# Optimization experiments

Hardware: AMD Instinct MI355X
Metric: run time of the kernel (lower is better)

The kernel has to match this reference:

```python
import jax, jax.numpy as jnp
import numpy as np
from jax import lax

B, C, H, W = 2, 128, 96, 96
K = 3
KK = K * K
EPS = 1e-5


def setup_inputs() -> dict:
    key = jax.random.key(0)
    ks = jax.random.split(key, 4)
    d = {"hu": jax.random.normal(ks[0], (B, C, H, W), jnp.float32)}
    for i in range(3):
        k = jax.random.split(ks[i + 1], 7)
        d["off_w%d" % (i + 1)] = jax.random.normal(k[0], (3 * KK, C, K, K), jnp.float32) * 0.01
        d["off_b%d" % (i + 1)] = jax.random.normal(k[1], (3 * KK,), jnp.float32) * 0.01
        d["w%d" % (i + 1)] = jax.random.normal(k[2], (C, C, K, K), jnp.float32) / np.float32(np.sqrt(C * KK))
        d["g%d" % (i + 1)] = jax.random.uniform(k[3], (C,), jnp.float32) + 0.5
        d["b%d" % (i + 1)] = jax.random.normal(k[4], (C,), jnp.float32) * 0.1
        d["m%d" % (i + 1)] = jax.random.normal(k[5], (C,), jnp.float32) * 0.1
        d["v%d" % (i + 1)] = jax.random.uniform(k[6], (C,), jnp.float32) + 0.5
    return d


def _mod_deform_conv(x, w, offset, mask, dilation):
    # x: [B,C,H,W]; offset: [B,2*KK,H,W] (dy,dx interleaved per kernel tap);
    # mask: [B,KK,H,W] (already sigmoid'ed). Zero padding outside the image.
    Hh, Ww = x.shape[2], x.shape[3]
    pad = dilation * (K - 1) // 2
    ky = jnp.repeat(jnp.arange(K), K).astype(x.dtype)  # [KK] row of each tap
    kx = jnp.tile(jnp.arange(K), K).astype(x.dtype)    # [KK] col of each tap
    gy = (jnp.arange(Hh, dtype=x.dtype) - pad)[None, :, None] + (ky * dilation)[:, None, None]  # [KK,H,1]
    gx = (jnp.arange(Ww, dtype=x.dtype) - pad)[None, None, :] + (kx * dilation)[:, None, None]  # [KK,1,W]
    off = offset.reshape(x.shape[0], KK, 2, Hh, Ww)
    py = gy[None] + off[:, :, 0]  # [B,KK,H,W] sampling row
    px = gx[None] + off[:, :, 1]  # [B,KK,H,W] sampling col

    def sample_one(xb, pyb, pxb, mb):
        # xb: [C,H,W]; pyb/pxb/mb: [KK,H,W]
        y0 = jnp.floor(pyb)
        x0 = jnp.floor(pxb)
        ly = pyb - y0
        lx = pxb - x0
        acc = jnp.zeros((xb.shape[0],) + pyb.shape, xb.dtype)
        for dy, wy in ((0, 1.0 - ly), (1, ly)):
            for dx, wx in ((0, 1.0 - lx), (1, lx)):
                yi = y0 + dy
                xi = x0 + dx
                valid = (yi >= 0) & (yi <= Hh - 1) & (xi >= 0) & (xi <= Ww - 1)
                yc = jnp.clip(yi, 0, Hh - 1).astype(jnp.int32)
                xc = jnp.clip(xi, 0, Ww - 1).astype(jnp.int32)
                v = xb[:, yc, xc]  # gather -> [C,KK,H,W]
                acc = acc + v * (wy * wx * valid.astype(xb.dtype))[None]
        return acc * mb[None]  # modulation

    sampled = jax.vmap(sample_one)(x, py, px, mask)  # [B,C,KK,H,W]
    return jnp.einsum('bckhw,ock->bohw', sampled, w.reshape(w.shape[0], w.shape[1], KK))


def _block(x, off_w, off_b, w, g, b, m, v, dilation):
    pad = dilation * (K - 1) // 2
    om = lax.conv_general_dilated(
        x, off_w, (1, 1), [(pad, pad), (pad, pad)],
        rhs_dilation=(dilation, dilation),
        dimension_numbers=('NCHW', 'OIHW', 'NCHW')) + off_b[None, :, None, None]
    offset = om[:, :2 * KK]
    mask = jax.nn.sigmoid(om[:, 2 * KK:])
    y = _mod_deform_conv(x, w, offset, mask, dilation)
    scale = (g / jnp.sqrt(v + EPS))[None, :, None, None]  # BN (inference form)
    y = (y - m[None, :, None, None]) * scale + b[None, :, None, None]
    return jax.nn.relu(y)


def reference(hu, off_w1, off_b1, w1, g1, b1, m1, v1,
              off_w2, off_b2, w2, g2, b2, m2, v2,
              off_w3, off_b3, w3, g3, b3, m3, v3):
    a1 = _block(hu, off_w1, off_b1, w1, g1, b1, m1, v1, 2) + hu
    a2 = _block(a1, off_w2, off_b2, w2, g2, b2, m2, v2, 4) + a1
    a3 = _block(a2, off_w3, off_b3, w3, g3, b3, m3, v3, 8) + a2
    return a3
```

## Files before the change

kernel.cpp:

```cpp
#include <hip/hip_runtime.h>
#include <math.h>

constexpr int Bn  = 2;
constexpr int Cn  = 128;
constexpr int Hn  = 96;
constexpr int Wn  = 96;
constexpr int HWn = Hn * Wn;
constexpr int CHWn = Cn * HWn;
constexpr int KCn = Cn * 9;
constexpr float EPSn = 1e-5f;
constexpr int KPAD = 1160;

typedef short bf16x8 __attribute__((ext_vector_type(8)));
typedef float f32x4  __attribute__((ext_vector_type(4)));

static __device__ inline short f2bf(float f) {
    union { float f; unsigned u; } v; v.f = f;
    unsigned r = v.u + 0x7fff + ((v.u >> 16) & 1);
    return (short)(r >> 16);
}
static __device__ inline unsigned pack2(float a, float b) {
    unsigned r;
    asm("v_cvt_pk_bf16_f32 %0, %1, %2" : "=v"(r) : "v"(a), "v"(b));
    return r;
}
static __device__ inline float bflo(unsigned u) { return __int_as_float(u << 16); }
static __device__ inline float bfhi(unsigned u) { return __int_as_float(u & 0xffff0000u); }

__global__ __launch_bounds__(256) void cvt_w_all(
    const float* __restrict__ w1, const float* __restrict__ w2,
    const float* __restrict__ w3, short* __restrict__ wbs)
{
    const int bid = blockIdx.x;
    const int stage = bid / 576;
    const float* w = (stage == 0) ? w1 : (stage == 1) ? w2 : w3;
    int t = (bid - stage * 576) * 256 + threadIdx.x;
    int e = t & 7, l = (t >> 3) & 63, rest = t >> 9;
    int j = rest % 36, g = rest / 36;
    int lr = l & 15, lq = l >> 4;
    int o = g * 16 + lr;
    int kidx = j * 32 + lq * 8 + e;
    int k = kidx >> 7, c = kidx & 127;
    wbs[stage * Cn * KCn + t] = f2bf(w[o * KCn + c * 9 + k]);
}

__global__ __launch_bounds__(256) void cvt_ow_all(
    const float* __restrict__ w1, const float* __restrict__ w2,
    const float* __restrict__ w3, short* __restrict__ owbs)
{
    const int bid = blockIdx.x;
    const int stage = bid / 144;
    const float* ow = (stage == 0) ? w1 : (stage == 1) ? w2 : w3;
    int t = (bid - stage * 144) * 256 + threadIdx.x;
    int e = t & 7, l = (t >> 3) & 63, rest = t >> 9;
    int kk = rest % 9, wvv = rest / 9;
    int mh = wvv & 1, ks = wvv >> 1;
    int lr = l & 15, lq = l >> 4;
    int o = mh * 16 + lr;
    int kidx = ks * 288 + kk * 32 + lq * 8 + e;
    int k = kidx >> 7, c = kidx & 127;
    owbs[stage * 32 * KCn + t] = (o < 27) ? f2bf(ow[o * KCn + c * 9 + k]) : (short)0;
}

__global__ __launch_bounds__(256) void nchw2nhwc(
    const float* __restrict__ x, unsigned short* __restrict__ xTb)
{
    __shared__ float Tl[128][65];
    const int t = threadIdx.x;
    const int pix0 = blockIdx.x * 64;
    const int b   = pix0 / HWn;
    const int sp0 = pix0 - b * HWn;
    const float* xb = x + b * CHWn + sp0 + (t & 63);
    const int c0 = t >> 6;
#pragma unroll 8
    for (int i = 0; i < 32; ++i) {
        const int c = c0 + 4 * i;
        Tl[c][t & 63] = xb[c * HWn];
    }
    __syncthreads();
    unsigned short* dstb = xTb + pix0 * 128;
#pragma unroll 8
    for (int i = 0; i < 32; ++i) {
        const int o = t + 256 * i;
        dstb[o] = (unsigned short)f2bf(Tl[o & 127][o >> 7]);
    }
}

__global__ __launch_bounds__(512, 6) void fused_stage(
    const unsigned short* __restrict__ xTb,
    const short* __restrict__ wbs, const short* __restrict__ owbs,
    const float* __restrict__ obv,
    const float* __restrict__ gv, const float* __restrict__ bv,
    const float* __restrict__ mv, const float* __restrict__ vv,
    unsigned short* __restrict__ outTb,
    float* __restrict__ outC, int dil, int last)
{
    __shared__ short S[16 * KPAD];
    __shared__ float offL[16][18];
    __shared__ float maskL[16][9];

    const int t   = threadIdx.x;
    const int l   = t & 63;
    const int wv  = t >> 6;
    const int lh  = l >> 5;
    const int lc  = l & 31;

    const int bid = blockIdx.x;
    const int swz = (bid & 7) * 144 + (bid >> 3);
    const int pix0 = swz * 16;
    const int b   = pix0 / HWn;
    const int sp0 = pix0 - b * HWn;
    const int hy  = sp0 / Wn;
    const int wx0 = sp0 - hy * Wn;
    const int basep = b * HWn;

    bf16x8 oaf[9];
    {
        const short* oarow = owbs + (wv * 9) * 512 + l * 8;
#pragma unroll
        for (int u = 0; u < 9; ++u) oaf[u] = *(const bf16x8*)(oarow + u * 512);
    }

#pragma unroll
    for (int bch = 0; bch < 3; ++bch) {
        uint2 vle[3];
#pragma unroll
        for (int u = 0; u < 3; ++u) {
            const int k  = bch * 3 + u;
            const int pp = wv * 2 + lh;
            const int iy = hy + (k / 3 - 1) * dil;
            const int ix = wx0 + pp + (k % 3 - 1) * dil;
            const bool v = (iy >= 0) && (iy < Hn) && (ix >= 0) && (ix < Wn);
            const int aof = v ? (basep + iy * Wn + ix) : basep;
            uint2 val = ((const uint2*)(xTb + aof * 128))[lc];
            vle[u].x = v ? val.x : 0u;
            vle[u].y = v ? val.y : 0u;
        }
#pragma unroll
        for (int u = 0; u < 3; ++u) {
            const int k  = bch * 3 + u;
            const int pp = wv * 2 + lh;
            ((uint2*)&S[pp * KPAD + k * 128])[lc] = vle[u];
        }
    }
    __syncthreads();

    f32x4 oacc = {0.f, 0.f, 0.f, 0.f};
    {
        const int ks = wv >> 1;
        const short* srow = &S[(l & 15) * KPAD + ks * 288 + ((l >> 4) * 8)];
#pragma unroll
        for (int bch = 0; bch < 3; ++bch) {
            bf16x8 bf[3];
#pragma unroll
            for (int u = 0; u < 3; ++u) bf[u] = *(const bf16x8*)(srow + (bch * 3 + u) * 32);
#pragma unroll
            for (int u = 0; u < 3; ++u)
                oacc = __builtin_amdgcn_mfma_f32_16x16x32_bf16(oaf[bch * 3 + u], bf[u], oacc, 0, 0, 0);
        }
    }
    __syncthreads();
    float* red = (float*)S;
    *(f32x4*)&red[wv * 256 + l * 4] = oacc;
    __syncthreads();
    if (wv < 2) {
        f32x4 s0 = *(const f32x4*)&red[(0 * 2 + wv) * 256 + l * 4];
        f32x4 s1 = *(const f32x4*)&red[(1 * 2 + wv) * 256 + l * 4];
        f32x4 s2 = *(const f32x4*)&red[(2 * 2 + wv) * 256 + l * 4];
        f32x4 s3 = *(const f32x4*)&red[(3 * 2 + wv) * 256 + l * 4];
        f32x4 sm = (s0 + s1) + (s2 + s3);
#pragma unroll
        for (int r = 0; r < 4; ++r) {
            int oc = wv * 16 + ((l >> 4) << 2) + r;
            if (oc < 18) {
                offL[l & 15][oc] = sm[r] + obv[oc];
            } else if (oc < 27) {
                float z = sm[r] + obv[oc];
                maskL[l & 15][oc - 18] = 1.f / (1.f + expf(-z));
            }
        }
    }
    __syncthreads();

    int pw0i = 0, pw1i = 0, pw2i = 0, pw3i = 0, pa0 = 0, pa1 = 0, pdx = 0;
    if (l < 18) {
        const int p = wv * 2 + l / 9;
        const int k = l - 9 * (l / 9);
        const float offy = offL[p][2 * k];
        const float offx = offL[p][2 * k + 1];
        const float m    = maskL[p][k];
        const float py = (float)(hy + (k / 3 - 1) * dil) + offy;
        const float px = (float)(wx0 + p + (k % 3 - 1) * dil) + offx;
        const float y0f = floorf(py), x0f = floorf(px);
        const float ly = py - y0f, lx = px - x0f;
        const int y0 = (int)y0f, x0 = (int)x0f;
        const float yv0 = (y0 >= 0 && y0 < Hn)      ? 1.f : 0.f;
        const float yv1 = (y0 >= -1 && y0 < Hn - 1) ? 1.f : 0.f;
        const float xv0 = (x0 >= 0 && x0 < Wn)      ? 1.f : 0.f;
        const float xv1 = (x0 >= -1 && x0 < Wn - 1) ? 1.f : 0.f;
        const float wy0 = (1.f - ly) * yv0 * m;
        const float wy1 = ly * yv1 * m;
        const float wxa = (1.f - lx) * xv0;
        const float wxb = lx * xv1;
        pw0i = __float_as_int(wy0 * wxa);
        pw1i = __float_as_int(wy0 * wxb);
        pw2i = __float_as_int(wy1 * wxa);
        pw3i = __float_as_int(wy1 * wxb);
        const int y0c = min(max(y0, 0), Hn - 1), y1c = min(max(y0 + 1, 0), Hn - 1);
        const int x0c = min(max(x0, 0), Wn - 1), x1c = min(max(x0 + 1, 0), Wn - 1);
        pa0 = (basep + y0c * Wn + x0c) * 128;
        pa1 = (basep + y1c * Wn + x1c) * 128;
        pdx = (x1c - x0c) * 128;
    }

    bf16x8 daf[6];
    {
        const short* darow = wbs + (wv * 36) * 512 + l * 8;
#pragma unroll
        for (int u = 0; u < 6; ++u) daf[u] = *(const bf16x8*)(darow + u * 512);
    }
    const int pp  = l & 15;
    const int ocb = wv * 16 + ((l >> 4) << 2);
    uint2 resb;
    if (last) {
        resb = *(const uint2*)&xTb[(pix0 + pp) * 128 + ocb];
    } else {
        const int o = t * 4;
        resb = *(const uint2*)&xTb[(pix0 + (o >> 7)) * 128 + (o & 127)];
    }

#pragma unroll
    for (int bch = 0; bch < 6; ++bch) {
        unsigned u00[3], u01[3], u10[3], u11[3];
        float    w00[3], w01[3], w10[3], w11[3];
#pragma unroll
        for (int u = 0; u < 3; ++u) {
            const int i = bch * 3 + u;
            w00[u] = __int_as_float(__builtin_amdgcn_readlane(pw0i, i));
            w01[u] = __int_as_float(__builtin_amdgcn_readlane(pw1i, i));
            w10[u] = __int_as_float(__builtin_amdgcn_readlane(pw2i, i));
            w11[u] = __int_as_float(__builtin_amdgcn_readlane(pw3i, i));
            const int a00 = __builtin_amdgcn_readlane(pa0, i);
            const int a11 = __builtin_amdgcn_readlane(pa1, i);
            const int dxk = __builtin_amdgcn_readlane(pdx, i);
            const unsigned short* xp = xTb + a00;
            const unsigned short* xq = xTb + a11;
            u00[u] = ((const unsigned*)xp)[l];
            u01[u] = ((const unsigned*)(xp + dxk))[l];
            u10[u] = ((const unsigned*)(xq - dxk))[l];
            u11[u] = ((const unsigned*)xq)[l];
        }
#pragma unroll
        for (int u = 0; u < 3; ++u) {
            const int i  = bch * 3 + u;
            const int di = i / 9;
            const int k  = i - di * 9;
            const int ppw = wv * 2 + di;
            float s0 = w00[u] * bflo(u00[u]) + w01[u] * bflo(u01[u])
                     + w10[u] * bflo(u10[u]) + w11[u] * bflo(u11[u]);
            float s1 = w00[u] * bfhi(u00[u]) + w01[u] * bfhi(u01[u])
                     + w10[u] * bfhi(u10[u]) + w11[u] * bfhi(u11[u]);
            ((unsigned*)&S[ppw * KPAD + k * 128])[l] = pack2(s0, s1);
        }
    }
    __syncthreads();

    f32x4 dacc = {0.f, 0.f, 0.f, 0.f};
    {
        const short* darow = wbs + (wv * 36) * 512 + l * 8;
        const short* srow  = &S[(l & 15) * KPAD + ((l >> 4) * 8)];
        {
            bf16x8 bf[6];
#pragma unroll
            for (int u = 0; u < 6; ++u) bf[u] = *(const bf16x8*)(srow + u * 32);
#pragma unroll
            for (int u = 0; u < 6; ++u)
                dacc = __builtin_amdgcn_mfma_f32_16x16x32_bf16(daf[u], bf[u], dacc, 0, 0, 0);
        }
#pragma unroll
        for (int bch = 1; bch < 6; ++bch) {
            bf16x8 af[6], bf[6];
#pragma unroll
            for (int u = 0; u < 6; ++u) af[u] = *(const bf16x8*)(darow + (bch * 6 + u) * 512);
#pragma unroll
            for (int u = 0; u < 6; ++u) bf[u] = *(const bf16x8*)(srow  + (bch * 6 + u) * 32);
#pragma unroll
            for (int u = 0; u < 6; ++u)
                dacc = __builtin_amdgcn_mfma_f32_16x16x32_bf16(af[u], bf[u], dacc, 0, 0, 0);
        }
    }

    if (last) {
        const float rs[4] = {bflo(resb.x), bfhi(resb.x), bflo(resb.y), bfhi(resb.y)};
#pragma unroll
        for (int r = 0; r < 4; ++r) {
            const int oc = ocb + r;
            const float sc = gv[oc] * rsqrtf(vv[oc] + EPSn);
            float y = (dacc[r] - mv[oc]) * sc + bv[oc];
            y = fmaxf(y, 0.f) + rs[r];
            outC[b * CHWn + oc * HWn + sp0 + pp] = y;
        }
    } else {
        __syncthreads();
        float* O = (float*)S;
#pragma unroll
        for (int r = 0; r < 4; ++r) {
            const int oc = ocb + r;
            const float sc = gv[oc] * rsqrtf(vv[oc] + EPSn);
            float y = (dacc[r] - mv[oc]) * sc + bv[oc];
            O[pp * 132 + oc] = fmaxf(y, 0.f);
        }
        __syncthreads();
        const int o  = t * 4;
        const int qp = o >> 7, qc = o & 127;
        f32x4 yv = *(f32x4*)&O[qp * 132 + qc];
        yv[0] += bflo(resb.x);
        yv[1] += bfhi(resb.x);
        yv[2] += bflo(resb.y);
        yv[3] += bfhi(resb.y);
        uint2 pk;
        pk.x = pack2(yv[0], yv[1]);
        pk.y = pack2(yv[2], yv[3]);
        *(uint2*)&outTb[(pix0 + qp) * 128 + qc] = pk;
    }
}

extern "C" void kernel_launch(void* const* d_in, const int* in_sizes, int n_in,
                              void* d_out, int out_size, void* d_ws, size_t ws_size,
                              hipStream_t stream) {
    (void)in_sizes; (void)n_in; (void)out_size; (void)ws_size;

    const float* hu = (const float*)d_in[0];

    short* wbs  = (short*)d_ws;
    short* owbs = wbs + 3 * Cn * KCn;
    unsigned short* T0b = (unsigned short*)(owbs + 3 * 32 * KCn);
    unsigned short* T1b = T0b + Bn * CHWn;

    cvt_w_all<<<3 * 576, 256, 0, stream>>>(
        (const float*)d_in[3], (const float*)d_in[10], (const float*)d_in[17], wbs);
    cvt_ow_all<<<3 * 144, 256, 0, stream>>>(
        (const float*)d_in[1], (const float*)d_in[8], (const float*)d_in[15], owbs);

    nchw2nhwc<<<(Bn * HWn) / 64, 256, 0, stream>>>(hu, T0b);

    const int dils[3] = {2, 4, 8};
    const unsigned short* insb[3] = {T0b, T1b, T0b};
    unsigned short* outsb[3] = {T1b, T0b, nullptr};
    const int nblk = (Bn * HWn) / 16;

    for (int i = 0; i < 3; ++i) {
        const float* obv = (const float*)d_in[2 + 7 * i];
        const float* gv  = (const float*)d_in[4 + 7 * i];
        const float* bv  = (const float*)d_in[5 + 7 * i];
        const float* mv  = (const float*)d_in[6 + 7 * i];
        const float* vv  = (const float*)d_in[7 + 7 * i];
        const int last = (i == 2);

        fused_stage<<<nblk, 512, 0, stream>>>(
            insb[i], wbs + i * Cn * KCn, owbs + i * 32 * KCn, obv,
            gv, bv, mv, vv, outsb[i],
            last ? (float*)d_out : nullptr, dils[i], last);
    }
}
```

Before: 106.3 us.

## Merge prep kernels into one launch and raise fused stage occupancy to 8

The two weight-conversion kernels and the NCHW-to-NHWC transpose are folded into a single prep kernel that branches on block index, cutting two launches. The fused stage kernel moves from launch bounds (512,6) to (512,8). To fit the tighter register budget it preloads fewer offset-conv and deform-conv weight fragments into registers and loads the rest just before use. This trades some extra load latency near the MFMAs for more resident waves. The merged prep kernel also allocates the transpose's shared tile for every block, which may reduce how many weight-conversion blocks fit per CU.

```diff
diff --git a/kernel.cpp b/kernel.cpp
--- a/kernel.cpp
+++ b/kernel.cpp
@@ -27,66 +27,64 @@
 static __device__ inline float bflo(unsigned u) { return __int_as_float(u << 16); }
 static __device__ inline float bfhi(unsigned u) { return __int_as_float(u & 0xffff0000u); }
 
-__global__ __launch_bounds__(256) void cvt_w_all(
+__global__ __launch_bounds__(256) void prep_all(
+    const float* __restrict__ hu,
     const float* __restrict__ w1, const float* __restrict__ w2,
-    const float* __restrict__ w3, short* __restrict__ wbs)
-{
-    const int bid = blockIdx.x;
-    const int stage = bid / 576;
-    const float* w = (stage == 0) ? w1 : (stage == 1) ? w2 : w3;
-    int t = (bid - stage * 576) * 256 + threadIdx.x;
-    int e = t & 7, l = (t >> 3) & 63, rest = t >> 9;
-    int j = rest % 36, g = rest / 36;
-    int lr = l & 15, lq = l >> 4;
-    int o = g * 16 + lr;
-    int kidx = j * 32 + lq * 8 + e;
-    int k = kidx >> 7, c = kidx & 127;
-    wbs[stage * Cn * KCn + t] = f2bf(w[o * KCn + c * 9 + k]);
-}
-
-__global__ __launch_bounds__(256) void cvt_ow_all(
-    const float* __restrict__ w1, const float* __restrict__ w2,
-    const float* __restrict__ w3, short* __restrict__ owbs)
-{
-    const int bid = blockIdx.x;
-    const int stage = bid / 144;
-    const float* ow = (stage == 0) ? w1 : (stage == 1) ? w2 : w3;
-    int t = (bid - stage * 144) * 256 + threadIdx.x;
-    int e = t & 7, l = (t >> 3) & 63, rest = t >> 9;
-    int kk = rest % 9, wvv = rest / 9;
-    int mh = wvv & 1, ks = wvv >> 1;
-    int lr = l & 15, lq = l >> 4;
-    int o = mh * 16 + lr;
-    int kidx = ks * 288 + kk * 32 + lq * 8 + e;
-    int k = kidx >> 7, c = kidx & 127;
-    owbs[stage * 32 * KCn + t] = (o < 27) ? f2bf(ow[o * KCn + c * 9 + k]) : (short)0;
-}
-
-__global__ __launch_bounds__(256) void nchw2nhwc(
-    const float* __restrict__ x, unsigned short* __restrict__ xTb)
+    const float* __restrict__ w3,
+    const float* __restrict__ o1, const float* __restrict__ o2,
+    const float* __restrict__ o3,
+    short* __restrict__ wbs, short* __restrict__ owbs,
+    unsigned short* __restrict__ xTb)
 {
     __shared__ float Tl[128][65];
-    const int t = threadIdx.x;
-    const int pix0 = blockIdx.x * 64;
-    const int b   = pix0 / HWn;
-    const int sp0 = pix0 - b * HWn;
-    const float* xb = x + b * CHWn + sp0 + (t & 63);
-    const int c0 = t >> 6;
+    const int bid = blockIdx.x;
+    if (bid < 1728) {
+        const int stage = bid / 576;
+        const float* w = (stage == 0) ? w1 : (stage == 1) ? w2 : w3;
+        int t = (bid - stage * 576) * 256 + threadIdx.x;
+        int e = t & 7, l = (t >> 3) & 63, rest = t >> 9;
+        int j = rest % 36, g = rest / 36;
+        int lr = l & 15, lq = l >> 4;
+        int o = g * 16 + lr;
+        int kidx = j * 32 + lq * 8 + e;
+        int k = kidx >> 7, c = kidx & 127;
+        wbs[stage * Cn * KCn + t] = f2bf(w[o * KCn + c * 9 + k]);
+    } else if (bid < 2160) {
+        const int rb = bid - 1728;
+        const int stage = rb / 144;
+        const float* ow = (stage == 0) ? o1 : (stage == 1) ? o2 : o3;
+        int t = (rb - stage * 144) * 256 + threadIdx.x;
+        int e = t & 7, l = (t >> 3) & 63, rest = t >> 9;
+        int kk = rest % 9, wvv = rest / 9;
+        int mh = wvv & 1, ks = wvv >> 1;
+        int lr = l & 15, lq = l >> 4;
+        int o = mh * 16 + lr;
+        int kidx = ks * 288 + kk * 32 + lq * 8 + e;
+        int k = kidx >> 7, c = kidx & 127;
+        owbs[stage * 32 * KCn + t] = (o < 27) ? f2bf(ow[o * KCn + c * 9 + k]) : (short)0;
+    } else {
+        const int t = threadIdx.x;
+        const int pix0 = (bid - 2160) * 64;
+        const int b   = pix0 / HWn;
+        const int sp0 = pix0 - b * HWn;
+        const float* xb = hu + b * CHWn + sp0 + (t & 63);
+        const int c0 = t >> 6;
 #pragma unroll 8
-    for (int i = 0; i < 32; ++i) {
-        const int c = c0 + 4 * i;
-        Tl[c][t & 63] = xb[c * HWn];
-    }
-    __syncthreads();
-    unsigned short* dstb = xTb + pix0 * 128;
+        for (int i = 0; i < 32; ++i) {
+            const int c = c0 + 4 * i;
+            Tl[c][t & 63] = xb[c * HWn];
+        }
+        __syncthreads();
+        unsigned short* dstb = xTb + pix0 * 128;
 #pragma unroll 8
-    for (int i = 0; i < 32; ++i) {
-        const int o = t + 256 * i;
-        dstb[o] = (unsigned short)f2bf(Tl[o & 127][o >> 7]);
-    }
-}
-
-__global__ __launch_bounds__(512, 6) void fused_stage(
+        for (int i = 0; i < 32; ++i) {
+            const int o = t + 256 * i;
+            dstb[o] = (unsigned short)f2bf(Tl[o & 127][o >> 7]);
+        }
+    }
+}
+
+__global__ __launch_bounds__(512, 8) void fused_stage(
     const unsigned short* __restrict__ xTb,
     const short* __restrict__ wbs, const short* __restrict__ owbs,
     const float* __restrict__ obv,
@@ -114,11 +112,11 @@
     const int wx0 = sp0 - hy * Wn;
     const int basep = b * HWn;
 
-    bf16x8 oaf[9];
+    bf16x8 oaf[6];
     {
         const short* oarow = owbs + (wv * 9) * 512 + l * 8;
 #pragma unroll
-        for (int u = 0; u < 9; ++u) oaf[u] = *(const bf16x8*)(oarow + u * 512);
+        for (int u = 0; u < 6; ++u) oaf[u] = *(const bf16x8*)(oarow + u * 512);
     }
 
 #pragma unroll
@@ -148,15 +146,26 @@
     f32x4 oacc = {0.f, 0.f, 0.f, 0.f};
     {
         const int ks = wv >> 1;
-        const short* srow = &S[(l & 15) * KPAD + ks * 288 + ((l >> 4) * 8)];
-#pragma unroll
-        for (int bch = 0; bch < 3; ++bch) {
+        const short* oarow = owbs + (wv * 9) * 512 + l * 8;
+        const short* srow  = &S[(l & 15) * KPAD + ks * 288 + ((l >> 4) * 8)];
+#pragma unroll
+        for (int bch = 0; bch < 2; ++bch) {
             bf16x8 bf[3];
 #pragma unroll
             for (int u = 0; u < 3; ++u) bf[u] = *(const bf16x8*)(srow + (bch * 3 + u) * 32);
 #pragma unroll
             for (int u = 0; u < 3; ++u)
                 oacc = __builtin_amdgcn_mfma_f32_16x16x32_bf16(oaf[bch * 3 + u], bf[u], oacc, 0, 0, 0);
+        }
+        {
+            bf16x8 af[3], bf[3];
+#pragma unroll
+            for (int u = 0; u < 3; ++u) af[u] = *(const bf16x8*)(oarow + (6 + u) * 512);
+#pragma unroll
+            for (int u = 0; u < 3; ++u) bf[u] = *(const bf16x8*)(srow + (6 + u) * 32);
+#pragma unroll
+            for (int u = 0; u < 3; ++u)
+                oacc = __builtin_amdgcn_mfma_f32_16x16x32_bf16(af[u], bf[u], oacc, 0, 0, 0);
         }
     }
     __syncthreads();
@@ -213,11 +222,11 @@
         pdx = (x1c - x0c) * 128;
     }
 
-    bf16x8 daf[6];
+    bf16x8 daf[4];
     {
         const short* darow = wbs + (wv * 36) * 512 + l * 8;
 #pragma unroll
-        for (int u = 0; u < 6; ++u) daf[u] = *(const bf16x8*)(darow + u * 512);
+        for (int u = 0; u < 4; ++u) daf[u] = *(const bf16x8*)(darow + u * 512);
     }
     const int pp  = l & 15;
     const int ocb = wv * 16 + ((l >> 4) << 2);
@@ -270,12 +279,16 @@
         const short* darow = wbs + (wv * 36) * 512 + l * 8;
         const short* srow  = &S[(l & 15) * KPAD + ((l >> 4) * 8)];
         {
-            bf16x8 bf[6];
+            bf16x8 af45[2], bf[6];
+            af45[0] = *(const bf16x8*)(darow + 4 * 512);
+            af45[1] = *(const bf16x8*)(darow + 5 * 512);
 #pragma unroll
             for (int u = 0; u < 6; ++u) bf[u] = *(const bf16x8*)(srow + u * 32);
 #pragma unroll
-            for (int u = 0; u < 6; ++u)
+            for (int u = 0; u < 4; ++u)
                 dacc = __builtin_amdgcn_mfma_f32_16x16x32_bf16(daf[u], bf[u], dacc, 0, 0, 0);
+            dacc = __builtin_amdgcn_mfma_f32_16x16x32_bf16(af45[0], bf[4], dacc, 0, 0, 0);
+            dacc = __builtin_amdgcn_mfma_f32_16x16x32_bf16(af45[1], bf[5], dacc, 0, 0, 0);
         }
 #pragma unroll
         for (int bch = 1; bch < 6; ++bch) {
@@ -337,12 +350,11 @@
     unsigned short* T0b = (unsigned short*)(owbs + 3 * 32 * KCn);
     unsigned short* T1b = T0b + Bn * CHWn;
 
-    cvt_w_all<<<3 * 576, 256, 0, stream>>>(
-        (const float*)d_in[3], (const float*)d_in[10], (const float*)d_in[17], wbs);
-    cvt_ow_all<<<3 * 144, 256, 0, stream>>>(
-        (const float*)d_in[1], (const float*)d_in[8], (const float*)d_in[15], owbs);
-
-    nchw2nhwc<<<(Bn * HWn) / 64, 256, 0, stream>>>(hu, T0b);
+    prep_all<<<2448, 256, 0, stream>>>(
+        hu,
+        (const float*)d_in[3], (const float*)d_in[10], (const float*)d_in[17],
+        (const float*)d_in[1], (const float*)d_in[8], (const float*)d_in[15],
+        wbs, owbs, T0b);
 
     const int dils[3] = {2, 4, 8};
     const unsigned short* insb[3] = {T0b, T1b, T0b};
```

Result: faster. 100.7 us (-5.3%).
